# Optimization experiments

Hardware: AMD Instinct MI355X
Metric: run time of the kernel (lower is better)

Reference implementation:

```python
import jax, jax.numpy as jnp
import numpy as np

B, T, C = 1024, 512, 41


def setup_inputs() -> dict:
    key = jax.random.key(0)
    k1, k2, k3, k4 = jax.random.split(key, 4)
    x = jax.random.normal(k1, (B, T, C), dtype=jnp.float32)
    # torchcrf initializes all transition params uniform(-0.1, 0.1)
    start_transitions = jax.random.uniform(k2, (C,), minval=-0.1, maxval=0.1, dtype=jnp.float32)
    end_transitions = jax.random.uniform(k3, (C,), minval=-0.1, maxval=0.1, dtype=jnp.float32)
    transitions = jax.random.uniform(k4, (C, C), minval=-0.1, maxval=0.1, dtype=jnp.float32)
    return {"x": x, "start_transitions": start_transitions,
            "end_transitions": end_transitions, "transitions": transitions}


def reference(x, start_transitions, end_transitions, transitions):
    # Viterbi decode (torchcrf CRF.decode, batch_first, no mask -> full length)
    # x: [B, T, C] emissions
    score0 = start_transitions[None, :] + x[:, 0]  # [B, C]

    def step(score, emit_t):
        # score: [B, C] best score ending in each tag at time t
        # emit_t: [B, C] emissions at time t+1
        cand = score[:, :, None] + transitions[None, :, :] + emit_t[:, None, :]  # [B, Cprev, Cnext]
        best = jnp.max(cand, axis=1)      # [B, C]
        bp = jnp.argmax(cand, axis=1)     # [B, C] backpointer: best previous tag
        return best, bp

    emits = jnp.swapaxes(x[:, 1:], 0, 1)  # [T-1, B, C]
    final, bps = jax.lax.scan(step, score0, emits)
    final = final + end_transitions[None, :]  # [B, C]
    last_tag = jnp.argmax(final, axis=1)      # [B] tag at time T-1

    def back(tag, bp_t):
        # tag: [B] tag at time t+1; bp_t: [B, C] backpointers into time t
        prev = jnp.take_along_axis(bp_t, tag[:, None], axis=1)[:, 0]
        return prev, tag

    first_tag, tags_rest = jax.lax.scan(back, last_tag, bps, reverse=True)
    # tags_rest[t] is the tag at time t+1 (t = 0..T-2); first_tag is tag at time 0
    tags = jnp.concatenate([first_tag[:, None], jnp.swapaxes(tags_rest, 0, 1)], axis=1)  # [B, T]
    return tags.astype(jnp.int64)
```

## Files before the change

kernel.cpp:

```cpp
#include <hip/hip_runtime.h>

#define BB 1024
#define TT 512
#define CC 41

__global__ __launch_bounds__(64) void crf_viterbi_kernel(
    const float* __restrict__ x,
    const float* __restrict__ start_t,
    const float* __restrict__ end_t,
    const float* __restrict__ trans,
    int* __restrict__ out)
{
    __shared__ unsigned char bp_lds[(TT - 1) * CC];
    __shared__ int tags_lds[TT];

    const int b = blockIdx.x;
    const int lane = threadIdx.x;
    const bool active = lane < CC;
    const int c = active ? lane : (CC - 1);

    float trans_reg[CC];
    #pragma unroll
    for (int p = 0; p < CC; ++p) trans_reg[p] = trans[p * CC + c];

    const float* xb = x + (size_t)b * TT * CC;

    float myscore = start_t[c] + xb[c];

    float emit_cur = xb[1 * CC + c];
    float emit_nxt = xb[2 * CC + c];

    for (int t = 1; t < TT; ++t) {
        const int tf = (t + 2 < TT) ? (t + 2) : (TT - 1);
        const float emit_fut = xb[(size_t)tf * CC + c];

        float v[CC];
        int  ix[CC];
        #pragma unroll
        for (int p = 0; p < CC; ++p) {
            const float sp = __int_as_float(
                __builtin_amdgcn_readlane(__float_as_int(myscore), p));
            v[p]  = (sp + trans_reg[p]) + emit_cur;
            ix[p] = p;
        }

#define COMBINE(i, j) do { \
            if (v[(j)] > v[(i)]) { v[(i)] = v[(j)]; ix[(i)] = ix[(j)]; } \
        } while (0)
        #pragma unroll
        for (int i = 0; i < 20; ++i) COMBINE(2 * i, 2 * i + 1);
        #pragma unroll
        for (int i = 0; i < 10; ++i) COMBINE(4 * i, 4 * i + 2);
        #pragma unroll
        for (int i = 0; i < 5; ++i)  COMBINE(8 * i, 8 * i + 4);
        COMBINE(0, 8);
        COMBINE(16, 24);
        COMBINE(0, 16);
        COMBINE(32, 40);
        COMBINE(0, 32);
#undef COMBINE

        myscore = v[0];
        if (active) bp_lds[(t - 1) * CC + lane] = (unsigned char)ix[0];

        emit_cur = emit_nxt;
        emit_nxt = emit_fut;
    }

    const float fin = myscore + end_t[c];

    float bestv = __int_as_float(__builtin_amdgcn_readlane(__float_as_int(fin), 0));
    int tag = 0;
    #pragma unroll
    for (int i = 1; i < CC; ++i) {
        const float vi = __int_as_float(
            __builtin_amdgcn_readlane(__float_as_int(fin), i));
        if (vi > bestv) { bestv = vi; tag = i; }
    }

    __syncthreads();

    if (lane == 0) {
        tags_lds[TT - 1] = tag;
        int tg = tag;
        for (int t = TT - 1; t >= 1; --t) {
            tg = (int)bp_lds[(t - 1) * CC + tg];
            tags_lds[t - 1] = tg;
        }
    }
    __syncthreads();

    int* ob = out + (size_t)b * TT;
    for (int i = lane; i < TT; i += 64) ob[i] = tags_lds[i];
}

extern "C" void kernel_launch(void* const* d_in, const int* in_sizes, int n_in,
                              void* d_out, int out_size, void* d_ws, size_t ws_size,
                              hipStream_t stream) {
    (void)in_sizes; (void)n_in; (void)d_ws; (void)ws_size; (void)out_size;
    const float* x       = (const float*)d_in[0];
    const float* start_t = (const float*)d_in[1];
    const float* end_t   = (const float*)d_in[2];
    const float* trans   = (const float*)d_in[3];
    int* out = (int*)d_out;

    crf_viterbi_kernel<<<dim3(BB), dim3(64), 0, stream>>>(x, start_t, end_t, trans, out);
}
```

Baseline: 261.6 us.

## Split Viterbi max-reduction over previous tags across two wavefronts per batch

Each block now uses two wavefronts. Each wavefront reduces half of the previous-tag candidates (21 and 20), and the partial maxima and argmax are exchanged through double-buffered LDS with a barrier every timestep. This halves the per-step serial readlane/compare chain on the critical path. In exchange it adds a __syncthreads and LDS traffic to each of the 511 steps and doubles the thread count per block.

New measurement: 463.0 us. 77.0% more time.

```diff
diff --git a/kernel.cpp b/kernel.cpp
--- a/kernel.cpp
+++ b/kernel.cpp
@@ -1,10 +1,15 @@
 #include <hip/hip_runtime.h>
+#include <math.h>
 
 #define BB 1024
 #define TT 512
 #define CC 41
 
-__global__ __launch_bounds__(64) void crf_viterbi_kernel(
+__device__ __forceinline__ float rlane(float xv, int l) {
+    return __int_as_float(__builtin_amdgcn_readlane(__float_as_int(xv), l));
+}
+
+__global__ __launch_bounds__(128) void crf_viterbi_kernel(
     const float* __restrict__ x,
     const float* __restrict__ start_t,
     const float* __restrict__ end_t,
@@ -13,17 +18,23 @@
 {
     __shared__ unsigned char bp_lds[(TT - 1) * CC];
     __shared__ int tags_lds[TT];
+    __shared__ float exAv[2][CC];
+    __shared__ float exBv[2][CC];
+    __shared__ int   exBi[2][CC];
 
-    const int b = blockIdx.x;
-    const int lane = threadIdx.x;
+    const int tid  = threadIdx.x;
+    const int w    = tid >> 6;
+    const int lane = tid & 63;
     const bool active = lane < CC;
     const int c = active ? lane : (CC - 1);
 
-    float trans_reg[CC];
-    #pragma unroll
-    for (int p = 0; p < CC; ++p) trans_reg[p] = trans[p * CC + c];
+    const int p0 = w ? 21 : 0;
+    const int np = w ? 20 : 21;
 
-    const float* xb = x + (size_t)b * TT * CC;
+    float trans_reg[21];
+    for (int p = 0; p < np; ++p) trans_reg[p] = trans[(p0 + p) * CC + c];
+
+    const float* xb = x + (size_t)blockIdx.x * TT * CC;
 
     float myscore = start_t[c] + xb[c];
 
@@ -31,37 +42,55 @@
     float emit_nxt = xb[2 * CC + c];
 
     for (int t = 1; t < TT; ++t) {
+        const int buf = t & 1;
         const int tf = (t + 2 < TT) ? (t + 2) : (TT - 1);
         const float emit_fut = xb[(size_t)tf * CC + c];
 
-        float v[CC];
-        int  ix[CC];
-        #pragma unroll
-        for (int p = 0; p < CC; ++p) {
-            const float sp = __int_as_float(
-                __builtin_amdgcn_readlane(__float_as_int(myscore), p));
-            v[p]  = (sp + trans_reg[p]) + emit_cur;
-            ix[p] = p;
+        float v[21]; int ix[21];
+        if (w == 0) {
+            #pragma unroll
+            for (int p = 0; p < 21; ++p) {
+                const float sp = rlane(myscore, p);
+                v[p]  = (sp + trans_reg[p]) + emit_cur;
+                ix[p] = p;
+            }
+        } else {
+            #pragma unroll
+            for (int p = 0; p < 20; ++p) {
+                const float sp = rlane(myscore, 21 + p);
+                v[p]  = (sp + trans_reg[p]) + emit_cur;
+                ix[p] = 21 + p;
+            }
+            v[20] = -INFINITY;
+            ix[20] = 63;
         }
 
-#define COMBINE(i, j) do { \
-            if (v[(j)] > v[(i)]) { v[(i)] = v[(j)]; ix[(i)] = ix[(j)]; } \
-        } while (0)
+#define COMBINE(i, j) if (v[(j)] > v[(i)]) { v[(i)] = v[(j)]; ix[(i)] = ix[(j)]; }
         #pragma unroll
-        for (int i = 0; i < 20; ++i) COMBINE(2 * i, 2 * i + 1);
+        for (int i = 0; i < 10; ++i) { COMBINE(2 * i, 2 * i + 1) }
         #pragma unroll
-        for (int i = 0; i < 10; ++i) COMBINE(4 * i, 4 * i + 2);
-        #pragma unroll
-        for (int i = 0; i < 5; ++i)  COMBINE(8 * i, 8 * i + 4);
-        COMBINE(0, 8);
-        COMBINE(16, 24);
-        COMBINE(0, 16);
-        COMBINE(32, 40);
-        COMBINE(0, 32);
+        for (int i = 0; i < 5; ++i)  { COMBINE(4 * i, 4 * i + 2) }
+        COMBINE(0, 4) COMBINE(8, 12) COMBINE(16, 20)
+        COMBINE(0, 8)
+        COMBINE(0, 16)
 #undef COMBINE
 
-        myscore = v[0];
-        if (active) bp_lds[(t - 1) * CC + lane] = (unsigned char)ix[0];
+        if (active) {
+            if (w == 0) { exAv[buf][lane] = v[0]; }
+            else        { exBv[buf][lane] = v[0]; exBi[buf][lane] = ix[0]; }
+        }
+        __syncthreads();
+
+        float va, vb; int bi;
+        if (w == 0) { va = v[0];         vb = exBv[buf][c]; bi = exBi[buf][c]; }
+        else        { va = exAv[buf][c]; vb = v[0];         bi = ix[0]; }
+
+        myscore = (vb > va) ? vb : va;
+
+        if (w == 0 && active) {
+            const int bp = (vb > va) ? bi : ix[0];
+            bp_lds[(t - 1) * CC + lane] = (unsigned char)bp;
+        }
 
         emit_cur = emit_nxt;
         emit_nxt = emit_fut;
@@ -69,18 +98,17 @@
 
     const float fin = myscore + end_t[c];
 
-    float bestv = __int_as_float(__builtin_amdgcn_readlane(__float_as_int(fin), 0));
+    float bestv = rlane(fin, 0);
     int tag = 0;
     #pragma unroll
     for (int i = 1; i < CC; ++i) {
-        const float vi = __int_as_float(
-            __builtin_amdgcn_readlane(__float_as_int(fin), i));
+        const float vi = rlane(fin, i);
         if (vi > bestv) { bestv = vi; tag = i; }
     }
 
     __syncthreads();
 
-    if (lane == 0) {
+    if (tid == 0) {
         tags_lds[TT - 1] = tag;
         int tg = tag;
         for (int t = TT - 1; t >= 1; --t) {
@@ -90,8 +118,8 @@
     }
     __syncthreads();
 
-    int* ob = out + (size_t)b * TT;
-    for (int i = lane; i < TT; i += 64) ob[i] = tags_lds[i];
+    int* ob = out + (size_t)blockIdx.x * TT;
+    for (int i = tid; i < TT; i += 128) ob[i] = tags_lds[i];
 }
 
 extern "C" void kernel_launch(void* const* d_in, const int* in_sizes, int n_in,
@@ -104,5 +132,5 @@
     const float* trans   = (const float*)d_in[3];
     int* out = (int*)d_out;
 
-    crf_viterbi_kernel<<<dim3(BB), dim3(64), 0, stream>>>(x, start_t, end_t, trans, out);
+    crf_viterbi_kernel<<<dim3(BB), dim3(128), 0, stream>>>(x, start_t, end_t, trans, out);
 }
```

## Parallelize backtrace via segment anchors and use max-then-match argmax

Applied to the files above, without the earlier changes.

Replaces the compare-and-select argmax tree with a pure fmaxf reduction followed by an equality scan to recover the backpointer. During the forward pass each lane composes backpointers with ds_bpermute to record, for every 64-step segment, which tag at the segment start leads to each end tag. The serial 511-step single-lane backtrace becomes eight lanes each walking one 64-step segment from boundary tags resolved by readlane. This adds a bpermute per step to the forward loop in exchange for a shorter serial backtrace tail.

Result: slower. 329.9 us (+26.1%).

```diff
diff --git a/kernel.cpp b/kernel.cpp
--- a/kernel.cpp
+++ b/kernel.cpp
@@ -3,6 +3,10 @@
 #define BB 1024
 #define TT 512
 #define CC 41
+
+__device__ __forceinline__ float rlanef(float xv, int l) {
+    return __int_as_float(__builtin_amdgcn_readlane(__float_as_int(xv), l));
+}
 
 __global__ __launch_bounds__(64) void crf_viterbi_kernel(
     const float* __restrict__ x,
@@ -14,7 +18,6 @@
     __shared__ unsigned char bp_lds[(TT - 1) * CC];
     __shared__ int tags_lds[TT];
 
-    const int b = blockIdx.x;
     const int lane = threadIdx.x;
     const bool active = lane < CC;
     const int c = active ? lane : (CC - 1);
@@ -23,75 +26,102 @@
     #pragma unroll
     for (int p = 0; p < CC; ++p) trans_reg[p] = trans[p * CC + c];
 
-    const float* xb = x + (size_t)b * TT * CC;
+    const float* xb = x + (size_t)blockIdx.x * TT * CC;
 
     float myscore = start_t[c] + xb[c];
 
     float emit_cur = xb[1 * CC + c];
     float emit_nxt = xb[2 * CC + c];
 
-    for (int t = 1; t < TT; ++t) {
-        const int tf = (t + 2 < TT) ? (t + 2) : (TT - 1);
-        const float emit_fut = xb[(size_t)tf * CC + c];
+    int A[8];
 
-        float v[CC];
-        int  ix[CC];
-        #pragma unroll
-        for (int p = 0; p < CC; ++p) {
-            const float sp = __int_as_float(
-                __builtin_amdgcn_readlane(__float_as_int(myscore), p));
-            v[p]  = (sp + trans_reg[p]) + emit_cur;
-            ix[p] = p;
+    #pragma unroll
+    for (int k = 0; k < 8; ++k) {
+        int anchor = lane;
+        const int nj = (k < 7) ? 64 : 63;
+        #pragma unroll 2
+        for (int j = 0; j < nj; ++j) {
+            const int t = 64 * k + j + 1;
+            const int tf = (t + 2 < TT) ? (t + 2) : (TT - 1);
+            const float emit_fut = xb[(size_t)tf * CC + c];
+
+            float v[CC];
+            #pragma unroll
+            for (int p = 0; p < CC; ++p) {
+                const float sp = rlanef(myscore, p);
+                v[p] = (sp + trans_reg[p]) + emit_cur;
+            }
+
+            float w0[21];
+            #pragma unroll
+            for (int i = 0; i < 20; ++i) w0[i] = fmaxf(v[2 * i], v[2 * i + 1]);
+            w0[20] = v[40];
+            float w1[11];
+            #pragma unroll
+            for (int i = 0; i < 10; ++i) w1[i] = fmaxf(w0[2 * i], w0[2 * i + 1]);
+            w1[10] = w0[20];
+            float w2[6];
+            #pragma unroll
+            for (int i = 0; i < 5; ++i) w2[i] = fmaxf(w1[2 * i], w1[2 * i + 1]);
+            w2[5] = w1[10];
+            float w3a = fmaxf(w2[0], w2[1]);
+            float w3b = fmaxf(w2[2], w2[3]);
+            float w3c = fmaxf(w2[4], w2[5]);
+            const float m = fmaxf(fmaxf(w3a, w3b), w3c);
+
+            int bp = 40;
+            #pragma unroll
+            for (int p = 39; p >= 0; --p) bp = (v[p] == m) ? p : bp;
+
+            myscore = m;
+            if (active) bp_lds[(t - 1) * CC + lane] = (unsigned char)bp;
+
+            anchor = __builtin_amdgcn_ds_bpermute(bp << 2, anchor);
+
+            emit_cur = emit_nxt;
+            emit_nxt = emit_fut;
         }
-
-#define COMBINE(i, j) do { \
-            if (v[(j)] > v[(i)]) { v[(i)] = v[(j)]; ix[(i)] = ix[(j)]; } \
-        } while (0)
-        #pragma unroll
-        for (int i = 0; i < 20; ++i) COMBINE(2 * i, 2 * i + 1);
-        #pragma unroll
-        for (int i = 0; i < 10; ++i) COMBINE(4 * i, 4 * i + 2);
-        #pragma unroll
-        for (int i = 0; i < 5; ++i)  COMBINE(8 * i, 8 * i + 4);
-        COMBINE(0, 8);
-        COMBINE(16, 24);
-        COMBINE(0, 16);
-        COMBINE(32, 40);
-        COMBINE(0, 32);
-#undef COMBINE
-
-        myscore = v[0];
-        if (active) bp_lds[(t - 1) * CC + lane] = (unsigned char)ix[0];
-
-        emit_cur = emit_nxt;
-        emit_nxt = emit_fut;
+        A[k] = anchor;
     }
 
     const float fin = myscore + end_t[c];
 
-    float bestv = __int_as_float(__builtin_amdgcn_readlane(__float_as_int(fin), 0));
+    float bestv = rlanef(fin, 0);
     int tag = 0;
     #pragma unroll
     for (int i = 1; i < CC; ++i) {
-        const float vi = __int_as_float(
-            __builtin_amdgcn_readlane(__float_as_int(fin), i));
+        const float vi = rlanef(fin, i);
         if (vi > bestv) { bestv = vi; tag = i; }
     }
 
+    int bnd[9];
+    bnd[8] = tag;
+    #pragma unroll
+    for (int k = 7; k >= 0; --k)
+        bnd[k] = __builtin_amdgcn_readlane(A[k], bnd[k + 1]);
+
     __syncthreads();
 
-    if (lane == 0) {
-        tags_lds[TT - 1] = tag;
-        int tg = tag;
-        for (int t = TT - 1; t >= 1; --t) {
-            tg = (int)bp_lds[(t - 1) * CC + tg];
-            tags_lds[t - 1] = tg;
+    {
+        int tg = bnd[1];
+        #pragma unroll
+        for (int k = 1; k < 8; ++k) if (lane == k) tg = bnd[k + 1];
+
+        if (lane == 0) tags_lds[TT - 1] = bnd[8];
+        if (lane < 8) {
+            const int rbase = 64 * lane;
+            const int nj = (lane < 7) ? 64 : 63;
+            for (int j = nj - 1; j >= 0; --j) {
+                tg = (int)bp_lds[(rbase + j) * CC + tg];
+                tags_lds[rbase + j] = tg;
+            }
         }
     }
     __syncthreads();
 
-    int* ob = out + (size_t)b * TT;
-    for (int i = lane; i < TT; i += 64) ob[i] = tags_lds[i];
+    int* ob = out + (size_t)blockIdx.x * TT;
+    #pragma unroll
+    for (int i = 0; i < TT / 64; ++i) ob[lane + 64 * i] = tags_lds[lane + 64 * i];
 }
 
 extern "C" void kernel_launch(void* const* d_in, const int* in_sizes, int n_in,
```
